# Performance work log

Measured on AMD Instinct MI355X. Metric: run time of the kernel, lower is better.

## Reference

```python
import jax, jax.numpy as jnp
import numpy as np

MAX_DELTAS = 4  # number of concurrently loaded delta adapters


def _dequant(qw, qz, sc):
    """GPTQ-style 4-bit dequant with a single group (g_idx == 0).

    qw: [D, O, K//8] int32, 8 x 4-bit values packed along the input (K) dim.
    qz: [D, O//8, 1] int32, 8 x 4-bit zero points packed along the output dim.
    sc: [D, O, 1] float scales (one group).
    Returns dense delta weights [D, O, K].
    """
    shifts = jnp.arange(8, dtype=jnp.int32) * 4
    D, O, Kp = qw.shape
    w = ((qw[:, :, :, None] >> shifts) & 0xF).reshape(D, O, Kp * 8)   # [D,O,K]
    z = ((qz[:, :, 0][:, :, None] >> shifts) & 0xF).reshape(D, O)     # [D,O]
    return (w.astype(sc.dtype) - (z.astype(sc.dtype) + 1.0)[:, :, None]) * sc


def setup_inputs() -> dict:
    key = jax.random.key(0)
    ks = jax.random.split(key, 16)
    T, IN = 1024, 4096
    Q, KV = 4096, 1024  # 32 q-heads, 8 kv-heads, head_size 128
    OUT = Q + 2 * KV    # 6144
    D, PACK = MAX_DELTAS, 8
    IMAX = np.int32(2**31 - 1)
    return {
        "x": jax.random.normal(ks[0], (T, IN), dtype=jnp.float32),
        "w_base": jax.random.normal(ks[1], (OUT, IN), dtype=jnp.float32) * 0.02,
        "bias": jax.random.normal(ks[2], (OUT,), dtype=jnp.float32) * 0.02,
        "qweight_q": jax.random.randint(ks[3], (D, Q, IN // PACK), 0, IMAX, dtype=jnp.int32),
        "qweight_k": jax.random.randint(ks[4], (D, KV, IN // PACK), 0, IMAX, dtype=jnp.int32),
        "qweight_v": jax.random.randint(ks[5], (D, KV, IN // PACK), 0, IMAX, dtype=jnp.int32),
        "qzeros_q": jax.random.randint(ks[6], (D, Q // PACK, 1), 0, IMAX, dtype=jnp.int32),
        "qzeros_k": jax.random.randint(ks[7], (D, KV // PACK, 1), 0, IMAX, dtype=jnp.int32),
        "qzeros_v": jax.random.randint(ks[8], (D, KV // PACK, 1), 0, IMAX, dtype=jnp.int32),
        "scales_q": jax.random.uniform(ks[9], (D, Q, 1), dtype=jnp.float32) * 0.01,
        "scales_k": jax.random.uniform(ks[10], (D, KV, 1), dtype=jnp.float32) * 0.01,
        "scales_v": jax.random.uniform(ks[11], (D, KV, 1), dtype=jnp.float32) * 0.01,
        "indices": jax.random.randint(ks[12], (T,), 0, D, dtype=jnp.int32),
    }


def reference(x, w_base, bias, qweight_q, qweight_k, qweight_v,
              qzeros_q, qzeros_k, qzeros_v, scales_q, scales_k, scales_v,
              indices):
    # Base fused QKV projection.
    out = x @ w_base.T + bias  # [T, OUT]
    # Dequantize the three packed delta stacks and concatenate along out dim,
    # matching the (q, k, v) output_slices scatter of apply_delta.
    Wd = jnp.concatenate([
        _dequant(qweight_q, qzeros_q, scales_q),
        _dequant(qweight_k, qzeros_k, scales_k),
        _dequant(qweight_v, qzeros_v, scales_v),
    ], axis=1)  # [D, OUT, IN]
    # Per-token indexed delta matmul: token t uses adapter indices[t].
    for d in range(MAX_DELTAS):
        xm = jnp.where((indices == d)[:, None], x, 0.0)  # [T, IN]
        out = out + xm @ Wd[d].T
    return out
```

## Files before the change

kernel.cpp:

```cpp
#include <hip/hip_runtime.h>
#include <stdint.h>

#define T_TOK 1024
#define K_IN  4096
#define N_OUT 6144
#define N_Q   4096
#define N_KV  1024
#define N_D   4
#define KP    512

#define TM 256
#define TN 256
#define BK 64
#define KSPLIT 4
#define KCH (K_IN / KSPLIT)
#define NSTEPS (KCH / BK)
#define PM_MAX 2048
#define XP_ROWS 1792
#define MT (PM_MAX/TM)
#define NT (N_OUT/TN)
#define NBLK (NT * MT * KSPLIT)

typedef __attribute__((ext_vector_type(8)))  short  short8;
typedef __attribute__((ext_vector_type(4)))  float  float4v;
typedef __attribute__((ext_vector_type(4)))  float  f32x4;
typedef __attribute__((ext_vector_type(4)))  uint   u32x4;

__device__ __forceinline__ ushort f2bf(float f) {
    uint32_t u = __float_as_uint(f);
    u = (u + 0x7FFFu + ((u >> 16) & 1u)) >> 16;
    return (ushort)u;
}
__device__ __forceinline__ uint pack2(ushort a, ushort b) {
    return (uint)a | ((uint)b << 16);
}

__global__ void build_perm_kernel(const int* __restrict__ indices,
                                  int* __restrict__ perm,
                                  int* __restrict__ pofs) {
    __shared__ int cnt[N_D], cur[N_D], ps[N_D + 1];
    int tid = threadIdx.x;
    if (tid < N_D) { cnt[tid] = 0; cur[tid] = 0; }
    __syncthreads();
    for (int t = tid; t < T_TOK; t += blockDim.x) atomicAdd(&cnt[indices[t]], 1);
    for (int p = tid; p < PM_MAX; p += blockDim.x) perm[p] = -1;
    __syncthreads();
    if (tid == 0) {
        int run = 0;
        for (int d = 0; d < N_D; d++) { ps[d] = run; run += ((cnt[d] + TM - 1) / TM) * TM; }
        ps[N_D] = run;
        for (int d = 0; d <= N_D; d++) pofs[d] = ps[d];
    }
    __syncthreads();
    for (int t = tid; t < T_TOK; t += blockDim.x) {
        int d = indices[t];
        int r = atomicAdd(&cur[d], 1);
        perm[ps[d] + r] = t;
    }
}

__global__ void dequant_wall_kernel(const float* __restrict__ w_base,
                                    const int* __restrict__ qw_q, const int* __restrict__ qw_k, const int* __restrict__ qw_v,
                                    const int* __restrict__ qz_q, const int* __restrict__ qz_k, const int* __restrict__ qz_v,
                                    const float* __restrict__ sc_q, const float* __restrict__ sc_k, const float* __restrict__ sc_v,
                                    ushort* __restrict__ wall) {
    int id  = blockIdx.x * blockDim.x + threadIdx.x;
    int kq  = id & (KP - 1);
    int o   = id >> 9;

    const int* qw; const int* qz; const float* sc; int r, Osec;
    if (o < N_Q)            { qw = qw_q; qz = qz_q; sc = sc_q; r = o;                Osec = N_Q;  }
    else if (o < N_Q + N_KV){ qw = qw_k; qz = qz_k; sc = sc_k; r = o - N_Q;          Osec = N_KV; }
    else                    { qw = qw_v; qz = qz_v; sc = sc_v; r = o - (N_Q + N_KV); Osec = N_KV; }

    const f32x4* wbp = (const f32x4*)(w_base + (size_t)o * K_IN + (size_t)kq * 8);
    f32x4 wb0 = __builtin_nontemporal_load(wbp);
    f32x4 wb1 = __builtin_nontemporal_load(wbp + 1);
    float wb[8] = {wb0.x, wb0.y, wb0.z, wb0.w, wb1.x, wb1.y, wb1.z, wb1.w};

#pragma unroll
    for (int d = 0; d < N_D; d++) {
        int   q  = __builtin_nontemporal_load(qw + ((size_t)d * Osec + r) * KP + kq);
        int   zq = qz[(size_t)d * (Osec / 8) + (r >> 3)];
        float s  = sc[(size_t)d * Osec + r];
        float zs = (float)(((zq >> ((r & 7) * 4)) & 0xF) + 1) * s;

        ushort res[8];
#pragma unroll
        for (int j = 0; j < 8; j++) {
            float v = wb[j] + (float)((q >> (4 * j)) & 0xF) * s - zs;
            res[j] = f2bf(v);
        }
        u32x4 packv;
        packv.x = pack2(res[0], res[1]); packv.y = pack2(res[2], res[3]);
        packv.z = pack2(res[4], res[5]); packv.w = pack2(res[6], res[7]);
        *(u32x4*)(wall + ((size_t)d * N_OUT + o) * K_IN + (size_t)kq * 8) = packv;
    }
}

__global__ void build_xp_kernel(const float* __restrict__ x,
                                const int* __restrict__ perm,
                                ushort* __restrict__ xp) {
    int pm = blockIdx.x;
    int c0 = blockIdx.y * 2048 + threadIdx.x * 8;
    int tok = perm[pm];
    ushort res[8];
    if (tok < 0) {
#pragma unroll
        for (int j = 0; j < 8; j++) res[j] = 0;
    } else {
        const f32x4* src = (const f32x4*)(x + (size_t)tok * K_IN + c0);
        f32x4 a = __builtin_nontemporal_load(src);
        f32x4 b = __builtin_nontemporal_load(src + 1);
        float v[8] = {a.x, a.y, a.z, a.w, b.x, b.y, b.z, b.w};
#pragma unroll
        for (int j = 0; j < 8; j++) res[j] = f2bf(v[j]);
    }
    u32x4 packv;
    packv.x = pack2(res[0], res[1]); packv.y = pack2(res[2], res[3]);
    packv.z = pack2(res[4], res[5]); packv.w = pack2(res[6], res[7]);
    *(u32x4*)(xp + (size_t)pm * K_IN + c0) = packv;
}

__global__ void init_out_kernel(const float* __restrict__ bias,
                                float* __restrict__ out) {
    int id = blockIdx.x * blockDim.x + threadIdx.x;
    int n4 = id & (N_OUT / 4 - 1);
    int t  = id / (N_OUT / 4);
    float4 b = *(const float4*)(bias + n4 * 4);
    *(float4*)(out + (size_t)t * N_OUT + n4 * 4) = b;
}

__global__ __launch_bounds__(512, 1) void gemm_kernel(
    const ushort* __restrict__ xp, const ushort* __restrict__ wall,
    const int* __restrict__ perm, const int* __restrict__ pofs,
    float* __restrict__ out) {

    __shared__ ushort As[2][TM * BK];
    __shared__ ushort Bs[2][TN * BK];

    int lin  = blockIdx.x;
    int low3 = lin & 7, rest = lin >> 3;
    int j    = rest % (MT * KSPLIT), bq = rest / (MT * KSPLIT);
    int bn   = bq * 8 + low3;
    int bm   = j % MT, kz = j / MT;

    int m0 = bm * TM, n0 = bn * TN;
    int ptot = pofs[N_D];
    if (m0 >= ptot) return;
    int d = 0;
    while (d < N_D - 1 && m0 >= pofs[d + 1]) d++;

    const ushort* wsec = wall + (size_t)d * N_OUT * K_IN;

    int tid  = threadIdx.x;
    int lane = tid & 63;
    int wv   = tid >> 6;
    int wm   = (wv & 3) * 64;
    int wn   = (wv >> 2) * 128;
    int quad = lane >> 4;
    int l16  = lane & 15;
    int xa   = l16 & 7;

    const float4v zero4 = {0.f, 0.f, 0.f, 0.f};
    float4v acc[4][8];
#pragma unroll
    for (int i = 0; i < 4; i++)
#pragma unroll
        for (int jj = 0; jj < 8; jj++) acc[i][jj] = zero4;

    auto stage = [&](ushort* dstA, ushort* dstB, int k0) {
#pragma unroll
        for (int w = 0; w < 4; w++) {
            int p   = w * 512 + tid;
            int row = p >> 3;
            int ckl = (p & 7) ^ (row & 7);
            const ushort* ga = xp   + (size_t)(m0 + row) * K_IN + k0 + ckl * 8;
            const ushort* gb = wsec + (size_t)(n0 + row) * K_IN + k0 + ckl * 8;
            int base = (w * 512 + (tid & ~63)) * 8;
            __builtin_amdgcn_global_load_lds((const __attribute__((address_space(1))) void*)ga,
                                             (__attribute__((address_space(3))) void*)(dstA + base), 16, 0, 0);
            __builtin_amdgcn_global_load_lds((const __attribute__((address_space(1))) void*)gb,
                                             (__attribute__((address_space(3))) void*)(dstB + base), 16, 0, 0);
        }
    };

    int kbase = kz * KCH;
    int buf = 0;
    stage(As[0], Bs[0], kbase);
    __syncthreads();

    for (int s = 0; s < NSTEPS; s++) {
        if (s + 1 < NSTEPS) stage(As[1 - buf], Bs[1 - buf], kbase + (s + 1) * BK);

        const ushort* Ab = As[buf];
        const ushort* Bb = Bs[buf];
#pragma unroll
        for (int kk = 0; kk < BK; kk += 32) {
            int ckb = (kk >> 3) + quad;
            short8 a[4], b[8];
#pragma unroll
            for (int i = 0; i < 4; i++)
                a[i] = *(const short8*)(Ab + (wm + i * 16 + l16) * BK + (ckb ^ xa) * 8);
#pragma unroll
            for (int jj = 0; jj < 8; jj++)
                b[jj] = *(const short8*)(Bb + (wn + jj * 16 + l16) * BK + (ckb ^ xa) * 8);
#pragma unroll
            for (int i = 0; i < 4; i++)
#pragma unroll
                for (int jj = 0; jj < 8; jj++)
                    acc[i][jj] = __builtin_amdgcn_mfma_f32_16x16x32_bf16(a[i], b[jj], acc[i][jj], 0, 0, 0);
        }
        __syncthreads();
        buf ^= 1;
    }

#pragma unroll
    for (int i = 0; i < 4; i++) {
        int toks[4];
#pragma unroll
        for (int r = 0; r < 4; r++) toks[r] = perm[m0 + wm + i * 16 + quad * 4 + r];
#pragma unroll
        for (int jj = 0; jj < 8; jj++) {
            int col = n0 + wn + jj * 16 + l16;
#pragma unroll
            for (int r = 0; r < 4; r++) {
                int tok = toks[r];
                if (tok >= 0) atomicAdd(out + (size_t)tok * N_OUT + col, acc[i][jj][r]);
            }
        }
    }
}

extern "C" void kernel_launch(void* const* d_in, const int* in_sizes, int n_in,
                              void* d_out, int out_size, void* d_ws, size_t ws_size,
                              hipStream_t stream) {
    const float* x      = (const float*)d_in[0];
    const float* w_base = (const float*)d_in[1];
    const float* bias   = (const float*)d_in[2];
    const int*   qw_q   = (const int*)d_in[3];
    const int*   qw_k   = (const int*)d_in[4];
    const int*   qw_v   = (const int*)d_in[5];
    const int*   qz_q   = (const int*)d_in[6];
    const int*   qz_k   = (const int*)d_in[7];
    const int*   qz_v   = (const int*)d_in[8];
    const float* sc_q   = (const float*)d_in[9];
    const float* sc_k   = (const float*)d_in[10];
    const float* sc_v   = (const float*)d_in[11];
    const int*   indices= (const int*)d_in[12];
    float* out = (float*)d_out;

    char* ws = (char*)d_ws;
    ushort* wall = (ushort*)ws;
    size_t wall_bytes = (size_t)N_D * N_OUT * K_IN * 2;
    ushort* xp = (ushort*)(ws + wall_bytes);
    size_t xp_bytes = (size_t)XP_ROWS * K_IN * 2;
    int* perm = (int*)(ws + wall_bytes + xp_bytes);
    int* pofs = perm + PM_MAX;

    build_perm_kernel<<<1, 256, 0, stream>>>(indices, perm, pofs);
    dequant_wall_kernel<<<(N_OUT * KP) / 256, 256, 0, stream>>>(
        w_base, qw_q, qw_k, qw_v, qz_q, qz_k, qz_v, sc_q, sc_k, sc_v, wall);
    build_xp_kernel<<<dim3(XP_ROWS, 2), 256, 0, stream>>>(x, perm, xp);
    init_out_kernel<<<(T_TOK * N_OUT / 4) / 256, 256, 0, stream>>>(bias, out);
    gemm_kernel<<<NBLK, 512, 0, stream>>>(xp, wall, perm, pofs, out);
}
```

Before: 378.5 us.

## Fuse 4-bit delta dequant into GEMM B-operand load and switch to fp16

```diff
diff --git a/kernel.cpp b/kernel.cpp
--- a/kernel.cpp
+++ b/kernel.cpp
@@ -1,4 +1,5 @@
 #include <hip/hip_runtime.h>
+#include <hip/hip_fp16.h>
 #include <stdint.h>
 
 #define T_TOK 1024
@@ -15,24 +16,20 @@
 #define KSPLIT 4
 #define KCH (K_IN / KSPLIT)
 #define NSTEPS (KCH / BK)
-#define PM_MAX 2048
-#define XP_ROWS 1792
+#define PM_MAX 1792
 #define MT (PM_MAX/TM)
 #define NT (N_OUT/TN)
 #define NBLK (NT * MT * KSPLIT)
 
-typedef __attribute__((ext_vector_type(8)))  short  short8;
-typedef __attribute__((ext_vector_type(4)))  float  float4v;
-typedef __attribute__((ext_vector_type(4)))  float  f32x4;
-typedef __attribute__((ext_vector_type(4)))  uint   u32x4;
-
-__device__ __forceinline__ ushort f2bf(float f) {
-    uint32_t u = __float_as_uint(f);
-    u = (u + 0x7FFFu + ((u >> 16) & 1u)) >> 16;
-    return (ushort)u;
-}
-__device__ __forceinline__ uint pack2(ushort a, ushort b) {
-    return (uint)a | ((uint)b << 16);
+typedef __attribute__((ext_vector_type(8))) _Float16 half8;
+typedef __attribute__((ext_vector_type(4))) float    float4v;
+typedef __attribute__((ext_vector_type(4))) float    f32x4;
+typedef __attribute__((ext_vector_type(4))) uint     u32x4;
+
+__device__ __forceinline__ uint packh2(float a, float b) {
+    union { __half2 h; uint u; } r;
+    r.h = __halves2half2(__float2half(a), __float2half(b));
+    return r.u;
 }
 
 __global__ void build_perm_kernel(const int* __restrict__ indices,
@@ -59,66 +56,51 @@
     }
 }
 
-__global__ void dequant_wall_kernel(const float* __restrict__ w_base,
-                                    const int* __restrict__ qw_q, const int* __restrict__ qw_k, const int* __restrict__ qw_v,
-                                    const int* __restrict__ qz_q, const int* __restrict__ qz_k, const int* __restrict__ qz_v,
-                                    const float* __restrict__ sc_q, const float* __restrict__ sc_k, const float* __restrict__ sc_v,
-                                    ushort* __restrict__ wall) {
-    int id  = blockIdx.x * blockDim.x + threadIdx.x;
-    int kq  = id & (KP - 1);
-    int o   = id >> 9;
-
-    const int* qw; const int* qz; const float* sc; int r, Osec;
-    if (o < N_Q)            { qw = qw_q; qz = qz_q; sc = sc_q; r = o;                Osec = N_Q;  }
-    else if (o < N_Q + N_KV){ qw = qw_k; qz = qz_k; sc = sc_k; r = o - N_Q;          Osec = N_KV; }
-    else                    { qw = qw_v; qz = qz_v; sc = sc_v; r = o - (N_Q + N_KV); Osec = N_KV; }
-
-    const f32x4* wbp = (const f32x4*)(w_base + (size_t)o * K_IN + (size_t)kq * 8);
-    f32x4 wb0 = __builtin_nontemporal_load(wbp);
-    f32x4 wb1 = __builtin_nontemporal_load(wbp + 1);
-    float wb[8] = {wb0.x, wb0.y, wb0.z, wb0.w, wb1.x, wb1.y, wb1.z, wb1.w};
-
-#pragma unroll
-    for (int d = 0; d < N_D; d++) {
-        int   q  = __builtin_nontemporal_load(qw + ((size_t)d * Osec + r) * KP + kq);
-        int   zq = qz[(size_t)d * (Osec / 8) + (r >> 3)];
-        float s  = sc[(size_t)d * Osec + r];
-        float zs = (float)(((zq >> ((r & 7) * 4)) & 0xF) + 1) * s;
-
-        ushort res[8];
-#pragma unroll
-        for (int j = 0; j < 8; j++) {
-            float v = wb[j] + (float)((q >> (4 * j)) & 0xF) * s - zs;
-            res[j] = f2bf(v);
-        }
-        u32x4 packv;
-        packv.x = pack2(res[0], res[1]); packv.y = pack2(res[2], res[3]);
-        packv.z = pack2(res[4], res[5]); packv.w = pack2(res[6], res[7]);
-        *(u32x4*)(wall + ((size_t)d * N_OUT + o) * K_IN + (size_t)kq * 8) = packv;
-    }
+__global__ void conv_wb_kernel(const float* __restrict__ w_base,
+                               __half* __restrict__ wb16) {
+    size_t id = (size_t)blockIdx.x * blockDim.x + threadIdx.x;
+    const f32x4* src = (const f32x4*)(w_base + id * 8);
+    f32x4 a = __builtin_nontemporal_load(src);
+    f32x4 b = __builtin_nontemporal_load(src + 1);
+    u32x4 packv;
+    packv.x = packh2(a.x, a.y); packv.y = packh2(a.z, a.w);
+    packv.z = packh2(b.x, b.y); packv.w = packh2(b.z, b.w);
+    *(u32x4*)(wb16 + id * 8) = packv;
+}
+
+__global__ void scaleprep_kernel(const int* __restrict__ qz_q, const int* __restrict__ qz_k, const int* __restrict__ qz_v,
+                                 const float* __restrict__ sc_q, const float* __restrict__ sc_k, const float* __restrict__ sc_v,
+                                 __half* __restrict__ sArr, __half* __restrict__ uArr) {
+    int id = blockIdx.x * blockDim.x + threadIdx.x;
+    int o  = id % N_OUT;
+    int d  = id / N_OUT;
+    const int* qz; const float* sc; int r, Osec;
+    if (o < N_Q)            { qz = qz_q; sc = sc_q; r = o;                Osec = N_Q;  }
+    else if (o < N_Q + N_KV){ qz = qz_k; sc = sc_k; r = o - N_Q;          Osec = N_KV; }
+    else                    { qz = qz_v; sc = sc_v; r = o - (N_Q + N_KV); Osec = N_KV; }
+    float s = sc[(size_t)d * Osec + r];
+    int  zq = qz[(size_t)d * (Osec / 8) + (r >> 3)];
+    int   z = (zq >> ((r & 7) * 4)) & 0xF;
+    sArr[id] = __float2half(s);
+    uArr[id] = __float2half((float)(z + 1) * s);
 }
 
 __global__ void build_xp_kernel(const float* __restrict__ x,
                                 const int* __restrict__ perm,
-                                ushort* __restrict__ xp) {
+                                __half* __restrict__ xp) {
     int pm = blockIdx.x;
     int c0 = blockIdx.y * 2048 + threadIdx.x * 8;
     int tok = perm[pm];
-    ushort res[8];
+    u32x4 packv;
     if (tok < 0) {
-#pragma unroll
-        for (int j = 0; j < 8; j++) res[j] = 0;
+        packv.x = packv.y = packv.z = packv.w = 0;
     } else {
         const f32x4* src = (const f32x4*)(x + (size_t)tok * K_IN + c0);
         f32x4 a = __builtin_nontemporal_load(src);
         f32x4 b = __builtin_nontemporal_load(src + 1);
-        float v[8] = {a.x, a.y, a.z, a.w, b.x, b.y, b.z, b.w};
-#pragma unroll
-        for (int j = 0; j < 8; j++) res[j] = f2bf(v[j]);
-    }
-    u32x4 packv;
-    packv.x = pack2(res[0], res[1]); packv.y = pack2(res[2], res[3]);
-    packv.z = pack2(res[4], res[5]); packv.w = pack2(res[6], res[7]);
+        packv.x = packh2(a.x, a.y); packv.y = packh2(a.z, a.w);
+        packv.z = packh2(b.x, b.y); packv.w = packh2(b.z, b.w);
+    }
     *(u32x4*)(xp + (size_t)pm * K_IN + c0) = packv;
 }
 
@@ -131,13 +113,34 @@
     *(float4*)(out + (size_t)t * N_OUT + n4 * 4) = b;
 }
 
-__global__ __launch_bounds__(512, 1) void gemm_kernel(
-    const ushort* __restrict__ xp, const ushort* __restrict__ wall,
+__device__ __forceinline__ half8 dq8(uint q, half8 wbf, __half2 s2, __half2 u2, __half2 h1024) {
+    union { half8 v; uint u[4]; } in, out;
+    in.v = wbf;
+    uint p[4];
+    p[0] = (q & 0xFu)         | ((q << 12) & 0xF0000u) | 0x64006400u;
+    p[1] = ((q >> 8) & 0xFu)  | ((q << 4)  & 0xF0000u) | 0x64006400u;
+    p[2] = ((q >> 16) & 0xFu) | ((q >> 4)  & 0xF0000u) | 0x64006400u;
+    p[3] = ((q >> 24) & 0xFu) | ((q >> 12) & 0xF0000u) | 0x64006400u;
+#pragma unroll
+    for (int i = 0; i < 4; i++) {
+        union { uint u; __half2 h; } qa, wa, ra;
+        qa.u = p[i]; wa.u = in.u[i];
+        ra.h = __hfma2(__hsub2(qa.h, h1024), s2, __hsub2(wa.h, u2));
+        out.u[i] = ra.u;
+    }
+    return out.v;
+}
+
+__global__ __launch_bounds__(512, 2) void gemm_kernel(
+    const __half* __restrict__ xp, const __half* __restrict__ wb16,
+    const int* __restrict__ qw_q, const int* __restrict__ qw_k, const int* __restrict__ qw_v,
+    const __half* __restrict__ sArr, const __half* __restrict__ uArr,
     const int* __restrict__ perm, const int* __restrict__ pofs,
     float* __restrict__ out) {
 
-    __shared__ ushort As[2][TM * BK];
-    __shared__ ushort Bs[2][TN * BK];
+    __shared__ __half As[2][TM * BK];
+    __shared__ __half Ws[2][TN * BK];
+    __shared__ int    Qs[2][TN * 8];
 
     int lin  = blockIdx.x;
     int low3 = lin & 7, rest = lin >> 3;
@@ -151,7 +154,12 @@
     int d = 0;
     while (d < N_D - 1 && m0 >= pofs[d + 1]) d++;
 
-    const ushort* wsec = wall + (size_t)d * N_OUT * K_IN;
+    const int* qwsec; int r0;
+    if (n0 < N_Q)             { qwsec = qw_q + (size_t)d * N_Q  * KP; r0 = n0; }
+    else if (n0 < N_Q + N_KV) { qwsec = qw_k + (size_t)d * N_KV * KP; r0 = n0 - N_Q; }
+    else                      { qwsec = qw_v + (size_t)d * N_KV * KP; r0 = n0 - (N_Q + N_KV); }
+    const __half* sSec = sArr + (size_t)d * N_OUT + n0;
+    const __half* uSec = uArr + (size_t)d * N_OUT + n0;
 
     int tid  = threadIdx.x;
     int lane = tid & 63;
@@ -162,6 +170,16 @@
     int l16  = lane & 15;
     int xa   = l16 & 7;
 
+    const __half2 h1024 = __half2half2(__float2half(1024.0f));
+
+    __half2 s2[8], u2[8];
+#pragma unroll
+    for (int jj = 0; jj < 8; jj++) {
+        int r = wn + jj * 16 + l16;
+        s2[jj] = __half2half2(sSec[r]);
+        u2[jj] = __half2half2(uSec[r]);
+    }
+
     const float4v zero4 = {0.f, 0.f, 0.f, 0.f};
     float4v acc[4][8];
 #pragma unroll
@@ -169,47 +187,57 @@
 #pragma unroll
         for (int jj = 0; jj < 8; jj++) acc[i][jj] = zero4;
 
-    auto stage = [&](ushort* dstA, ushort* dstB, int k0) {
+    auto gll = [](const void* g, void* l) {
+        __builtin_amdgcn_global_load_lds((const __attribute__((address_space(1))) void*)g,
+                                         (__attribute__((address_space(3))) void*)l, 16, 0, 0);
+    };
+
+    auto stage = [&](int buf, int k0) {
+        __half* dA = As[buf]; __half* dW = Ws[buf]; int* dQ = Qs[buf];
 #pragma unroll
         for (int w = 0; w < 4; w++) {
             int p   = w * 512 + tid;
             int row = p >> 3;
             int ckl = (p & 7) ^ (row & 7);
-            const ushort* ga = xp   + (size_t)(m0 + row) * K_IN + k0 + ckl * 8;
-            const ushort* gb = wsec + (size_t)(n0 + row) * K_IN + k0 + ckl * 8;
             int base = (w * 512 + (tid & ~63)) * 8;
-            __builtin_amdgcn_global_load_lds((const __attribute__((address_space(1))) void*)ga,
-                                             (__attribute__((address_space(3))) void*)(dstA + base), 16, 0, 0);
-            __builtin_amdgcn_global_load_lds((const __attribute__((address_space(1))) void*)gb,
-                                             (__attribute__((address_space(3))) void*)(dstB + base), 16, 0, 0);
+            gll(xp   + (size_t)(m0 + row) * K_IN + k0 + ckl * 8, dA + base);
+            gll(wb16 + (size_t)(n0 + row) * K_IN + k0 + ckl * 8, dW + base);
+        }
+        {
+            int row = tid >> 1, hf = tid & 1;
+            gll(qwsec + (size_t)(r0 + row) * KP + (k0 >> 3) + hf * 4,
+                dQ + (size_t)(tid & ~63) * 4);
         }
     };
 
     int kbase = kz * KCH;
     int buf = 0;
-    stage(As[0], Bs[0], kbase);
+    stage(0, kbase);
     __syncthreads();
 
     for (int s = 0; s < NSTEPS; s++) {
-        if (s + 1 < NSTEPS) stage(As[1 - buf], Bs[1 - buf], kbase + (s + 1) * BK);
-
-        const ushort* Ab = As[buf];
-        const ushort* Bb = Bs[buf];
+        if (s + 1 < NSTEPS) stage(1 - buf, kbase + (s + 1) * BK);
+
+        const __half* Ab = As[buf];
+        const __half* Wb = Ws[buf];
+        const int*    Qb = Qs[buf];
 #pragma unroll
         for (int kk = 0; kk < BK; kk += 32) {
             int ckb = (kk >> 3) + quad;
-            short8 a[4], b[8];
+            half8 a[4];
 #pragma unroll
             for (int i = 0; i < 4; i++)
-                a[i] = *(const short8*)(Ab + (wm + i * 16 + l16) * BK + (ckb ^ xa) * 8);
-#pragma unroll
-            for (int jj = 0; jj < 8; jj++)
-                b[jj] = *(const short8*)(Bb + (wn + jj * 16 + l16) * BK + (ckb ^ xa) * 8);
-#pragma unroll
-            for (int i = 0; i < 4; i++)
-#pragma unroll
-                for (int jj = 0; jj < 8; jj++)
-                    acc[i][jj] = __builtin_amdgcn_mfma_f32_16x16x32_bf16(a[i], b[jj], acc[i][jj], 0, 0, 0);
+                a[i] = *(const half8*)(Ab + (wm + i * 16 + l16) * BK + (ckb ^ xa) * 8);
+#pragma unroll
+            for (int jj = 0; jj < 8; jj++) {
+                int   r   = wn + jj * 16 + l16;
+                half8 wbf = *(const half8*)(Wb + r * BK + (ckb ^ xa) * 8);
+                uint  q   = (uint)Qb[r * 8 + ckb];
+                half8 b   = dq8(q, wbf, s2[jj], u2[jj], h1024);
+#pragma unroll
+                for (int i = 0; i < 4; i++)
+                    acc[i][jj] = __builtin_amdgcn_mfma_f32_16x16x32_f16(a[i], b, acc[i][jj], 0, 0, 0);
+            }
         }
         __syncthreads();
         buf ^= 1;
@@ -251,17 +279,21 @@
     float* out = (float*)d_out;
 
     char* ws = (char*)d_ws;
-    ushort* wall = (ushort*)ws;
-    size_t wall_bytes = (size_t)N_D * N_OUT * K_IN * 2;
-    ushort* xp = (ushort*)(ws + wall_bytes);
-    size_t xp_bytes = (size_t)XP_ROWS * K_IN * 2;
-    int* perm = (int*)(ws + wall_bytes + xp_bytes);
+    __half* wb16 = (__half*)ws;
+    size_t wb_bytes = (size_t)N_OUT * K_IN * 2;
+    __half* xp = (__half*)(ws + wb_bytes);
+    size_t xp_bytes = (size_t)PM_MAX * K_IN * 2;
+    __half* sArr = (__half*)(ws + wb_bytes + xp_bytes);
+    __half* uArr = sArr + (size_t)N_D * N_OUT;
+    int* perm = (int*)(uArr + (size_t)N_D * N_OUT);
     int* pofs = perm + PM_MAX;
 
     build_perm_kernel<<<1, 256, 0, stream>>>(indices, perm, pofs);
-    dequant_wall_kernel<<<(N_OUT * KP) / 256, 256, 0, stream>>>(
-        w_base, qw_q, qw_k, qw_v, qz_q, qz_k, qz_v, sc_q, sc_k, sc_v, wall);
-    build_xp_kernel<<<dim3(XP_ROWS, 2), 256, 0, stream>>>(x, perm, xp);
+    conv_wb_kernel<<<(N_OUT * (K_IN / 8)) / 256, 256, 0, stream>>>(w_base, wb16);
+    scaleprep_kernel<<<(N_D * N_OUT) / 256, 256, 0, stream>>>(
+        qz_q, qz_k, qz_v, sc_q, sc_k, sc_v, sArr, uArr);
+    build_xp_kernel<<<dim3(PM_MAX, 2), 256, 0, stream>>>(x, perm, xp);
     init_out_kernel<<<(T_TOK * N_OUT / 4) / 256, 256, 0, stream>>>(bias, out);
-    gemm_kernel<<<NBLK, 512, 0, stream>>>(xp, wall, perm, pofs, out);
-}
+    gemm_kernel<<<NBLK, 512, 0, stream>>>(xp, wb16, qw_q, qw_k, qw_v,
+                                          sArr, uArr, perm, pofs, out);
+}
```

Measured after the change: 424.5 us. 1.12x slower.
